# Kernel optimization log

Measured on AMD Instinct MI355X. Metric: run time of the kernel, lower is better.

## Reference

```python
import jax, jax.numpy as jnp
import numpy as np

N = 131072          # total nodes
E = 4194304         # edges (avg degree 32)
SUB = 16            # size_subgraph_samples
HID = 256


def _gcn_norm(src, dst, n):
    # add self-loops
    loops = jnp.arange(n, dtype=src.dtype)
    src = jnp.concatenate([src, loops])
    dst = jnp.concatenate([dst, loops])
    deg = jax.ops.segment_sum(jnp.ones_like(dst, dtype=jnp.float32), dst, num_segments=n)
    dinv = jnp.where(deg > 0, jax.lax.rsqrt(deg), 0.0)
    norm = dinv[src] * dinv[dst]  # [E+N]
    return src, dst, norm


def _gcn_conv(x, W, b, src, dst, norm, n):
    h = x @ W                                  # [N, out]
    msg = h[src] * norm[:, None]               # gather + scale
    agg = jax.ops.segment_sum(msg, dst, num_segments=n)
    return agg + b


def setup_inputs() -> dict:
    key = jax.random.key(0)
    ks = jax.random.split(key, 6)
    x = jax.random.normal(ks[0], (N, 128), dtype=jnp.float32)
    edge_index = jax.random.randint(ks[1], (2, E), 0, N, dtype=jnp.int64)
    W1 = jax.random.normal(ks[2], (128, HID), dtype=jnp.float32) * (1.0 / np.sqrt(128))
    b1 = jnp.zeros((HID,), dtype=jnp.float32)
    W2 = jax.random.normal(ks[3], (HID, HID), dtype=jnp.float32) * (1.0 / np.sqrt(HID))
    b2 = jnp.zeros((HID,), dtype=jnp.float32)
    Wout = jax.random.normal(ks[4], (HID * SUB, 1), dtype=jnp.float32) * (1.0 / np.sqrt(HID * SUB))
    bout = jnp.zeros((1,), dtype=jnp.float32)
    return {"x": x, "edge_index": edge_index, "W1": W1, "b1": b1,
            "W2": W2, "b2": b2, "Wout": Wout, "bout": bout}


def reference(x, edge_index, W1, b1, W2, b2, Wout, bout):
    n = x.shape[0]
    src, dst, norm = _gcn_norm(edge_index[0], edge_index[1], n)
    h = jax.nn.relu(_gcn_conv(x, W1, b1, src, dst, norm, n))
    h = jax.nn.relu(_gcn_conv(h, W2, b2, src, dst, norm, n))
    h = h.reshape(n // SUB, SUB * h.shape[1])   # [8192, 4096]
    return h @ Wout + bout                       # [8192, 1]
```

## Files before the change

kernel.cpp:

```cpp
#include <hip/hip_runtime.h>
#include <stdint.h>

#define NN 131072
#define NE 4194304
#define BKT 256
#define BKT_SH 9
#define BCAP 20480

typedef __bf16 bf16x8 __attribute__((ext_vector_type(8)));
typedef float  floatx4 __attribute__((ext_vector_type(4)));
typedef unsigned short u16x8 __attribute__((ext_vector_type(8)));

__device__ __forceinline__ float bf2f(unsigned short u) {
  union { unsigned int i; float f; } v; v.i = ((unsigned int)u) << 16; return v.f;
}
__device__ __forceinline__ unsigned short f2bf(float f) {
  union { float f; unsigned int i; } v; v.f = f;
  unsigned int r = v.i + 0x7fffu + ((v.i >> 16) & 1u);
  return (unsigned short)(r >> 16);
}


__global__ __launch_bounds__(256) void k_bzero(int* __restrict__ bktCnt) {
  bktCnt[threadIdx.x] = 0;
}

__global__ __launch_bounds__(1024) void k_bucket(const int* __restrict__ src,
                                                 const int* __restrict__ dst,
                                                 int* __restrict__ bktCnt,
                                                 unsigned int* __restrict__ bktBuf) {
  __shared__ int hist[BKT];
  __shared__ int base[BKT];
  const int t = threadIdx.x;
  if (t < BKT) hist[t] = 0;
  __syncthreads();
  const int e0 = (blockIdx.x * 1024 + t);
  const int4 s = ((const int4*)src)[e0];
  const int4 d = ((const int4*)dst)[e0];
  const int b0 = ((unsigned)d.x) >> BKT_SH, b1 = ((unsigned)d.y) >> BKT_SH;
  const int b2 = ((unsigned)d.z) >> BKT_SH, b3 = ((unsigned)d.w) >> BKT_SH;
  const int r0 = atomicAdd(&hist[b0], 1);
  const int r1 = atomicAdd(&hist[b1], 1);
  const int r2 = atomicAdd(&hist[b2], 1);
  const int r3 = atomicAdd(&hist[b3], 1);
  __syncthreads();
  if (t < BKT) base[t] = atomicAdd(&bktCnt[t], hist[t]);
  __syncthreads();
  const unsigned p0 = (((unsigned)s.x) << BKT_SH) | (d.x & 511);
  const unsigned p1 = (((unsigned)s.y) << BKT_SH) | (d.y & 511);
  const unsigned p2 = (((unsigned)s.z) << BKT_SH) | (d.z & 511);
  const unsigned p3 = (((unsigned)s.w) << BKT_SH) | (d.w & 511);
  bktBuf[(size_t)b0 * BCAP + base[b0] + r0] = p0;
  bktBuf[(size_t)b1 * BCAP + base[b1] + r1] = p1;
  bktBuf[(size_t)b2 * BCAP + base[b2] + r2] = p2;
  bktBuf[(size_t)b3 * BCAP + base[b3] + r3] = p3;
}

__global__ __launch_bounds__(1024) void k_csr(const int* __restrict__ bktCnt,
                                              const unsigned int* __restrict__ bktBuf,
                                              int* __restrict__ row_ptr,
                                              float* __restrict__ dinv,
                                              int* __restrict__ csr) {
  __shared__ int bsum[BKT];
  __shared__ int hist[512];
  __shared__ int sc[512];
  __shared__ int cur[512];
  const int b = blockIdx.x;
  const int t = threadIdx.x;
  if (t < BKT) bsum[t] = bktCnt[t];
  if (t < 512) hist[t] = 0;
  __syncthreads();
  for (int off = 1; off < BKT; off <<= 1) {
    int v = 0;
    if (t < BKT && t >= off) v = bsum[t - off];
    __syncthreads();
    if (t < BKT) bsum[t] += v;
    __syncthreads();
  }
  const int sz = bktCnt[b];
  const int csrBase = bsum[b] - sz;
  const unsigned int* eb = bktBuf + (size_t)b * BCAP;
  for (int i = t; i < sz; i += 1024) atomicAdd(&hist[eb[i] & 511], 1);
  __syncthreads();
  if (t < 512) sc[t] = hist[t];
  __syncthreads();
  for (int off = 1; off < 512; off <<= 1) {
    int v = 0;
    if (t < 512 && t >= off) v = sc[t - off];
    __syncthreads();
    if (t < 512) sc[t] += v;
    __syncthreads();
  }
  if (t < 512) {
    const int ex = csrBase + sc[t] - hist[t];
    row_ptr[b * 512 + t] = ex;
    cur[t] = ex;
    dinv[b * 512 + t] = rsqrtf((float)(hist[t] + 1));
  }
  if (b == BKT - 1 && t == 0) row_ptr[NN] = NE;
  __syncthreads();
  for (int i = t; i < sz; i += 1024) {
    const unsigned e = eb[i];
    csr[atomicAdd(&cur[e & 511], 1)] = (int)(e >> BKT_SH);
  }
}

__global__ __launch_bounds__(256) void k_cvt(const float* __restrict__ X,
                                             unsigned short* __restrict__ Xb) {
  const int t = blockIdx.x * 256 + threadIdx.x;
  const float4 v = ((const float4*)X)[t];
  ushort4 o;
  o.x = f2bf(v.x); o.y = f2bf(v.y); o.z = f2bf(v.z); o.w = f2bf(v.w);
  ((ushort4*)Xb)[t] = o;
}

__global__ __launch_bounds__(256) void k_swizzle(const float* __restrict__ W,
                                                 unsigned short* __restrict__ Wsw) {
  const int t = blockIdx.x * 256 + threadIdx.x;
  const int k = t >> 8, n = t & 255;
  const int s = ((k >> 5) * 16 + (n >> 4)) * 512 + ((k >> 3) & 3) * 128 + (n & 15) * 8 + (k & 7);
  Wsw[s] = f2bf(W[t]);
}

__global__ __launch_bounds__(256) void agg_h(const unsigned short* __restrict__ X,
                                             const int* __restrict__ row_ptr,
                                             const int* __restrict__ csr,
                                             const float* __restrict__ dinv,
                                             unsigned short* __restrict__ Y,
                                             int F, int foff) {
  const int lane = threadIdx.x & 63;
  const int node = (blockIdx.x * blockDim.x + threadIdx.x) >> 6;
  const int sub = lane >> 4;
  const int fl = lane & 15;
  const int start = row_ptr[node];
  const int end = row_ptr[node + 1];
  const float di = dinv[node];
  float a[8] = {0.f, 0.f, 0.f, 0.f, 0.f, 0.f, 0.f, 0.f};
  const unsigned short* Xf = X + foff + fl * 8;

  for (int e = start; e < end; e += 64) {
    const int nload = min(end - e, 64);
    int s_l = node;
    float w_l = 0.0f;
    if (lane < nload) {
      s_l = __builtin_nontemporal_load(&csr[e + lane]);
      w_l = dinv[s_l];
    }
    for (int j = 0; j < nload; j += 16) {
      const int i0 = j + sub, i1 = j + 4 + sub, i2 = j + 8 + sub, i3 = j + 12 + sub;
      const int s0 = __shfl(s_l, i0); const float w0 = __shfl(w_l, i0);
      const int s1 = __shfl(s_l, i1); const float w1 = __shfl(w_l, i1);
      const int s2 = __shfl(s_l, i2); const float w2 = __shfl(w_l, i2);
      const int s3 = __shfl(s_l, i3); const float w3 = __shfl(w_l, i3);
      const u16x8 r0 = *(const u16x8*)(Xf + (size_t)s0 * F);
      const u16x8 r1 = *(const u16x8*)(Xf + (size_t)s1 * F);
      const u16x8 r2 = *(const u16x8*)(Xf + (size_t)s2 * F);
      const u16x8 r3 = *(const u16x8*)(Xf + (size_t)s3 * F);
#pragma unroll
      for (int i = 0; i < 8; ++i) a[i] = fmaf(w0, bf2f(r0[i]), a[i]);
#pragma unroll
      for (int i = 0; i < 8; ++i) a[i] = fmaf(w1, bf2f(r1[i]), a[i]);
#pragma unroll
      for (int i = 0; i < 8; ++i) a[i] = fmaf(w2, bf2f(r2[i]), a[i]);
#pragma unroll
      for (int i = 0; i < 8; ++i) a[i] = fmaf(w3, bf2f(r3[i]), a[i]);
    }
  }
#pragma unroll
  for (int i = 0; i < 8; ++i) a[i] += __shfl_xor(a[i], 16);
#pragma unroll
  for (int i = 0; i < 8; ++i) a[i] += __shfl_xor(a[i], 32);
  const u16x8 sv = *(const u16x8*)(Xf + (size_t)node * F);
#pragma unroll
  for (int i = 0; i < 8; ++i) a[i] = fmaf(di, bf2f(sv[i]), a[i]);
  if (sub == 0) {
    u16x8 o;
#pragma unroll
    for (int i = 0; i < 8; ++i) o[i] = f2bf(di * a[i]);
    *(u16x8*)(Y + (size_t)node * F + foff + fl * 8) = o;
  }
}

template <int K>
__global__ __launch_bounds__(512) void k_gemm(const unsigned short* __restrict__ A,
                                              const unsigned short* __restrict__ Wsw,
                                              const float* __restrict__ bias,
                                              unsigned short* __restrict__ out) {
  __shared__ unsigned short lW[128 * 256];
  const int tid = threadIdx.x;
  const int wave = tid >> 6;
  const int lane = tid & 63;
  const int q = lane >> 4;
  const int m16 = lane & 15;
  const size_t baseM = (size_t)blockIdx.x * 256;

  floatx4 acc[2][16];
#pragma unroll
  for (int t = 0; t < 2; ++t)
#pragma unroll
    for (int nt = 0; nt < 16; ++nt) acc[t][nt] = (floatx4){0.f, 0.f, 0.f, 0.f};

  const size_t rowA0 = baseM + wave * 32 + m16;
  const size_t rowA1 = rowA0 + 16;

  for (int half = 0; half < K / 128; ++half) {
    __syncthreads();
    const uint4* gsrc = (const uint4*)(Wsw + half * 32768);
    uint4* ldst = (uint4*)lW;
#pragma unroll
    for (int i = 0; i < 8; ++i) ldst[i * 512 + tid] = gsrc[i * 512 + tid];
    __syncthreads();

#pragma unroll
    for (int kc = 0; kc < 4; ++kc) {
      const int koff = half * 128 + kc * 32 + q * 8;
      const bf16x8 av0 = *(const bf16x8*)(A + rowA0 * K + koff);
      const bf16x8 av1 = *(const bf16x8*)(A + rowA1 * K + koff);
#pragma unroll
      for (int nt = 0; nt < 16; ++nt) {
        const bf16x8 bv = *(const bf16x8*)(&lW[(kc * 16 + nt) * 512 + lane * 8]);
        acc[0][nt] = __builtin_amdgcn_mfma_f32_16x16x32_bf16(av0, bv, acc[0][nt], 0, 0, 0);
        acc[1][nt] = __builtin_amdgcn_mfma_f32_16x16x32_bf16(av1, bv, acc[1][nt], 0, 0, 0);
      }
    }
  }
  const int rq = (lane >> 4) * 4;
#pragma unroll
  for (int t = 0; t < 2; ++t) {
#pragma unroll
    for (int nt = 0; nt < 16; ++nt) {
      const int col = nt * 16 + m16;
      const float bv = bias[col];
#pragma unroll
      for (int r = 0; r < 4; ++r) {
        const size_t row = baseM + wave * 32 + t * 16 + rq + r;
        float v = acc[t][nt][r] + bv;
        v = fmaxf(v, 0.0f);
        out[row * 256 + col] = f2bf(v);
      }
    }
  }
}

__global__ __launch_bounds__(512) void k_gemm_out(const unsigned short* __restrict__ A,
                                                  const unsigned short* __restrict__ Wsw,
                                                  const float* __restrict__ bias,
                                                  const float* __restrict__ Wout,
                                                  const float* __restrict__ bout,
                                                  float* __restrict__ out) {
  constexpr int K = 256;
  __shared__ unsigned short lW[128 * 256];
  const int tid = threadIdx.x;
  const int wave = tid >> 6;
  const int lane = tid & 63;
  const int q = lane >> 4;
  const int m16 = lane & 15;
  const size_t baseM = (size_t)blockIdx.x * 256;

  floatx4 acc[2][16];
#pragma unroll
  for (int t = 0; t < 2; ++t)
#pragma unroll
    for (int nt = 0; nt < 16; ++nt) acc[t][nt] = (floatx4){0.f, 0.f, 0.f, 0.f};

  const size_t rowA0 = baseM + wave * 32 + m16;
  const size_t rowA1 = rowA0 + 16;

  for (int half = 0; half < 2; ++half) {
    __syncthreads();
    const uint4* gsrc = (const uint4*)(Wsw + half * 32768);
    uint4* ldst = (uint4*)lW;
#pragma unroll
    for (int i = 0; i < 8; ++i) ldst[i * 512 + tid] = gsrc[i * 512 + tid];
    __syncthreads();

#pragma unroll
    for (int kc = 0; kc < 4; ++kc) {
      const int koff = half * 128 + kc * 32 + q * 8;
      const bf16x8 av0 = *(const bf16x8*)(A + rowA0 * K + koff);
      const bf16x8 av1 = *(const bf16x8*)(A + rowA1 * K + koff);
#pragma unroll
      for (int nt = 0; nt < 16; ++nt) {
        const bf16x8 bv = *(const bf16x8*)(&lW[(kc * 16 + nt) * 512 + lane * 8]);
        acc[0][nt] = __builtin_amdgcn_mfma_f32_16x16x32_bf16(av0, bv, acc[0][nt], 0, 0, 0);
        acc[1][nt] = __builtin_amdgcn_mfma_f32_16x16x32_bf16(av1, bv, acc[1][nt], 0, 0, 0);
      }
    }
  }
  const int rq = (lane >> 4) * 4;
  float p0 = 0.f, p1 = 0.f;
#pragma unroll
  for (int nt = 0; nt < 16; ++nt) {
    const int col = nt * 16 + m16;
    const float bv = bias[col];
#pragma unroll
    for (int r = 0; r < 4; ++r) {
      const float wv = Wout[(rq + r) * 256 + col];
      const float v0 = fmaxf(acc[0][nt][r] + bv, 0.0f);
      const float v1 = fmaxf(acc[1][nt][r] + bv, 0.0f);
      p0 = fmaf(v0, wv, p0);
      p1 = fmaf(v1, wv, p1);
    }
  }
#pragma unroll
  for (int off = 32; off > 0; off >>= 1) {
    p0 += __shfl_xor(p0, off);
    p1 += __shfl_xor(p1, off);
  }
  if (lane == 0) {
    const float bo = bout[0];
    const int g = blockIdx.x * 16 + wave * 2;
    out[g]     = p0 + bo;
    out[g + 1] = p1 + bo;
  }
}

extern "C" void kernel_launch(void* const* d_in, const int* in_sizes, int n_in,
                              void* d_out, int out_size, void* d_ws, size_t ws_size,
                              hipStream_t stream) {
  const float* x    = (const float*)d_in[0];
  const int*   ei   = (const int*)d_in[1];
  const float* W1   = (const float*)d_in[2];
  const float* b1   = (const float*)d_in[3];
  const float* W2   = (const float*)d_in[4];
  const float* b2   = (const float*)d_in[5];
  const float* Wout = (const float*)d_in[6];
  const float* bout = (const float*)d_in[7];
  float* out = (float*)d_out;

  char* ws = (char*)d_ws;
  size_t off = 0;
  auto alloc = [&](size_t bytes) {
    char* p = ws + off;
    off += (bytes + 511) & ~(size_t)511;
    return p;
  };
  int*            row_ptr = (int*)alloc(((size_t)NN + 1) * 4);
  float*          dinv    = (float*)alloc((size_t)NN * 4);
  int*            bktCnt  = (int*)alloc(BKT * 4);
  unsigned int*   bktBuf  = (unsigned int*)alloc((size_t)BKT * BCAP * 4);
  int*            csr     = (int*)alloc((size_t)NE * 4);
  unsigned short* Wsw1    = (unsigned short*)alloc(128 * 256 * 2);
  unsigned short* Wsw2    = (unsigned short*)alloc(256 * 256 * 2);
  unsigned short* xb      = (unsigned short*)alloc((size_t)NN * 128 * 2);
  unsigned short* bufA    = (unsigned short*)alloc((size_t)NN * 256 * 2);
  unsigned short* bufB    = (unsigned short*)alloc((size_t)NN * 256 * 2);
  (void)in_sizes; (void)n_in; (void)out_size; (void)ws_size;

  const int* src = ei;
  const int* dst = ei + NE;

  hipLaunchKernelGGL(k_bzero,  dim3(1), dim3(256), 0, stream, bktCnt);
  hipLaunchKernelGGL(k_bucket, dim3(NE / 4096), dim3(1024), 0, stream, src, dst, bktCnt, bktBuf);
  hipLaunchKernelGGL(k_csr,    dim3(BKT), dim3(1024), 0, stream, bktCnt, bktBuf, row_ptr, dinv, csr);
  hipLaunchKernelGGL(k_cvt,    dim3(NN * 128 / 4 / 256), dim3(256), 0, stream, x, xb);
  hipLaunchKernelGGL(k_swizzle, dim3(128), dim3(256), 0, stream, W1, Wsw1);
  hipLaunchKernelGGL(k_swizzle, dim3(256), dim3(256), 0, stream, W2, Wsw2);

  hipLaunchKernelGGL(agg_h, dim3(NN / 4), dim3(256), 0, stream, xb, row_ptr, csr, dinv, bufA, 128, 0);
  hipLaunchKernelGGL(k_gemm<128>, dim3(NN / 256), dim3(512), 0, stream, bufA, Wsw1, b1, bufB);
  hipLaunchKernelGGL(agg_h, dim3(NN / 4), dim3(256), 0, stream, bufB, row_ptr, csr, dinv, bufA, 256, 0);
  hipLaunchKernelGGL(agg_h, dim3(NN / 4), dim3(256), 0, stream, bufB, row_ptr, csr, dinv, bufA, 256, 128);
  hipLaunchKernelGGL(k_gemm_out, dim3(NN / 256), dim3(512), 0, stream, bufA, Wsw2, b2, Wout, bout, out);
}
```

Baseline: 710.1 us.

## Replicate CSR shared histograms, merge swizzle launches, split aggregation into node halves

The CSR build kernel now keeps two copies of the per-bucket histogram and cursor arrays, chosen by thread parity, to reduce shared-memory atomic contention. The two weight swizzle launches are merged into one kernel. Each aggregation launch is split into two launches covering the lower and upper halves of the nodes, adding a node_base parameter. The aggregation split adds launches and likely targets cache locality per half or probes timing, at the cost of extra launch overhead.

Measured after the change: 731.9 us. 1.03x slower.

```diff
diff --git a/kernel.cpp b/kernel.cpp
--- a/kernel.cpp
+++ b/kernel.cpp
@@ -62,13 +62,16 @@
                                               float* __restrict__ dinv,
                                               int* __restrict__ csr) {
   __shared__ int bsum[BKT];
-  __shared__ int hist[512];
+  __shared__ int histA[512];
+  __shared__ int histB[512];
   __shared__ int sc[512];
-  __shared__ int cur[512];
+  __shared__ int curA[512];
+  __shared__ int curB[512];
   const int b = blockIdx.x;
   const int t = threadIdx.x;
+  const int rep = t & 1;
   if (t < BKT) bsum[t] = bktCnt[t];
-  if (t < 512) hist[t] = 0;
+  if (t < 512) { histA[t] = 0; histB[t] = 0; }
   __syncthreads();
   for (int off = 1; off < BKT; off <<= 1) {
     int v = 0;
@@ -80,9 +83,10 @@
   const int sz = bktCnt[b];
   const int csrBase = bsum[b] - sz;
   const unsigned int* eb = bktBuf + (size_t)b * BCAP;
-  for (int i = t; i < sz; i += 1024) atomicAdd(&hist[eb[i] & 511], 1);
-  __syncthreads();
-  if (t < 512) sc[t] = hist[t];
+  for (int i = t; i < sz; i += 1024)
+    atomicAdd(rep ? &histB[eb[i] & 511] : &histA[eb[i] & 511], 1);
+  __syncthreads();
+  if (t < 512) sc[t] = histA[t] + histB[t];
   __syncthreads();
   for (int off = 1; off < 512; off <<= 1) {
     int v = 0;
@@ -92,16 +96,20 @@
     __syncthreads();
   }
   if (t < 512) {
-    const int ex = csrBase + sc[t] - hist[t];
+    const int cnt = histA[t] + histB[t];
+    const int ex = csrBase + sc[t] - cnt;
     row_ptr[b * 512 + t] = ex;
-    cur[t] = ex;
-    dinv[b * 512 + t] = rsqrtf((float)(hist[t] + 1));
+    curA[t] = ex;
+    curB[t] = ex + histA[t];
+    dinv[b * 512 + t] = rsqrtf((float)(cnt + 1));
   }
   if (b == BKT - 1 && t == 0) row_ptr[NN] = NE;
   __syncthreads();
   for (int i = t; i < sz; i += 1024) {
     const unsigned e = eb[i];
-    csr[atomicAdd(&cur[e & 511], 1)] = (int)(e >> BKT_SH);
+    const int n = e & 511;
+    const int pos = atomicAdd(rep ? &curB[n] : &curA[n], 1);
+    csr[pos] = (int)(e >> BKT_SH);
   }
 }
 
@@ -114,9 +122,14 @@
   ((ushort4*)Xb)[t] = o;
 }
 
-__global__ __launch_bounds__(256) void k_swizzle(const float* __restrict__ W,
-                                                 unsigned short* __restrict__ Wsw) {
-  const int t = blockIdx.x * 256 + threadIdx.x;
+__global__ __launch_bounds__(256) void k_swizzle2(const float* __restrict__ W1,
+                                                  unsigned short* __restrict__ Wsw1,
+                                                  const float* __restrict__ W2,
+                                                  unsigned short* __restrict__ Wsw2) {
+  int b = blockIdx.x;
+  const float* W; unsigned short* Wsw;
+  if (b < 128) { W = W1; Wsw = Wsw1; } else { W = W2; Wsw = Wsw2; b -= 128; }
+  const int t = b * 256 + threadIdx.x;
   const int k = t >> 8, n = t & 255;
   const int s = ((k >> 5) * 16 + (n >> 4)) * 512 + ((k >> 3) & 3) * 128 + (n & 15) * 8 + (k & 7);
   Wsw[s] = f2bf(W[t]);
@@ -127,9 +140,9 @@
                                              const int* __restrict__ csr,
                                              const float* __restrict__ dinv,
                                              unsigned short* __restrict__ Y,
-                                             int F, int foff) {
+                                             int F, int foff, int node_base) {
   const int lane = threadIdx.x & 63;
-  const int node = (blockIdx.x * blockDim.x + threadIdx.x) >> 6;
+  const int node = node_base + ((blockIdx.x * blockDim.x + threadIdx.x) >> 6);
   const int sub = lane >> 4;
   const int fl = lane & 15;
   const int start = row_ptr[node];
@@ -354,12 +367,14 @@
   hipLaunchKernelGGL(k_bucket, dim3(NE / 4096), dim3(1024), 0, stream, src, dst, bktCnt, bktBuf);
   hipLaunchKernelGGL(k_csr,    dim3(BKT), dim3(1024), 0, stream, bktCnt, bktBuf, row_ptr, dinv, csr);
   hipLaunchKernelGGL(k_cvt,    dim3(NN * 128 / 4 / 256), dim3(256), 0, stream, x, xb);
-  hipLaunchKernelGGL(k_swizzle, dim3(128), dim3(256), 0, stream, W1, Wsw1);
-  hipLaunchKernelGGL(k_swizzle, dim3(256), dim3(256), 0, stream, W2, Wsw2);
-
-  hipLaunchKernelGGL(agg_h, dim3(NN / 4), dim3(256), 0, stream, xb, row_ptr, csr, dinv, bufA, 128, 0);
+  hipLaunchKernelGGL(k_swizzle2, dim3(384), dim3(256), 0, stream, W1, Wsw1, W2, Wsw2);
+
+  hipLaunchKernelGGL(agg_h, dim3(NN / 8), dim3(256), 0, stream, xb, row_ptr, csr, dinv, bufA, 128, 0, 0);
+  hipLaunchKernelGGL(agg_h, dim3(NN / 8), dim3(256), 0, stream, xb, row_ptr, csr, dinv, bufA, 128, 0, NN / 2);
   hipLaunchKernelGGL(k_gemm<128>, dim3(NN / 256), dim3(512), 0, stream, bufA, Wsw1, b1, bufB);
-  hipLaunchKernelGGL(agg_h, dim3(NN / 4), dim3(256), 0, stream, bufB, row_ptr, csr, dinv, bufA, 256, 0);
-  hipLaunchKernelGGL(agg_h, dim3(NN / 4), dim3(256), 0, stream, bufB, row_ptr, csr, dinv, bufA, 256, 128);
+  hipLaunchKernelGGL(agg_h, dim3(NN / 8), dim3(256), 0, stream, bufB, row_ptr, csr, dinv, bufA, 256, 0, 0);
+  hipLaunchKernelGGL(agg_h, dim3(NN / 8), dim3(256), 0, stream, bufB, row_ptr, csr, dinv, bufA, 256, 0, NN / 2);
+  hipLaunchKernelGGL(agg_h, dim3(NN / 8), dim3(256), 0, stream, bufB, row_ptr, csr, dinv, bufA, 256, 128, 0);
+  hipLaunchKernelGGL(agg_h, dim3(NN / 8), dim3(256), 0, stream, bufB, row_ptr, csr, dinv, bufA, 256, 128, NN / 2);
   hipLaunchKernelGGL(k_gemm_out, dim3(NN / 256), dim3(512), 0, stream, bufA, Wsw2, b2, Wout, bout, out);
 }
```
